# Optimization experiments

Measured on AMD Instinct MI355X. Metric: run time of the kernel, lower is better.

The kernel has to match this reference:

```python
import jax, jax.numpy as jnp
import numpy as np

IN_FEATURES = 4096
OUT_FEATURES = 4096


def setup_inputs() -> dict:
    key = jax.random.key(0)
    k1, k2 = jax.random.split(key)
    x = jax.random.normal(k1, (4, 2048, IN_FEATURES), dtype=jnp.float32)
    latent_weight = jax.random.normal(k2, (OUT_FEATURES, IN_FEATURES), dtype=jnp.float32) * 0.02
    return {"x": x, "latent_weight": latent_weight}


def _quantize(w):
    # abs-mean scale, ternary {-alpha, 0, alpha} with threshold 0.5*alpha
    alpha = jnp.mean(jnp.abs(w))
    threshold = 0.5 * alpha
    return jnp.where(w > threshold, alpha, jnp.where(w < -threshold, -alpha, jnp.zeros_like(w)))


def reference(x, latent_weight):
    qw = _quantize(latent_weight.astype(jnp.float32))
    # F.linear: x @ qw.T  -> [B, S, out_features]
    out = jnp.einsum('bsi,oi->bso', x.astype(jnp.float32), qw)
    return out.astype(x.dtype)
```

## Files before the change

kernel.cpp:

```cpp
#include <hip/hip_runtime.h>
#include <hip/hip_bf16.h>
#include <stdint.h>

#define M_DIM 8192
#define K_DIM 4096
#define N_DIM 4096

typedef __attribute__((ext_vector_type(8))) short short8;
typedef __attribute__((ext_vector_type(4))) float f32x4;

__device__ __forceinline__ void lds_load16(const ushort* g, ushort* l) {
    __builtin_amdgcn_global_load_lds(
        (const __attribute__((address_space(1))) uint32_t*)g,
        (__attribute__((address_space(3))) uint32_t*)l, 16, 0, 0);
}

__device__ __forceinline__ ushort f2bf_rne(float f) {
    uint32_t u = __float_as_uint(f);
    uint32_t r = (u + 0x7FFFu + ((u >> 16) & 1u)) >> 16;
    return (ushort)r;
}

__global__ void k_prep(const float* __restrict__ w, double* __restrict__ partial,
                       const float* __restrict__ x, ushort* __restrict__ xb) {
    const int nth = gridDim.x * blockDim.x;
    const int gtid = blockIdx.x * blockDim.x + threadIdx.x;

    const float4* w4 = (const float4*)w;
    double s = 0.0;
    for (int i = gtid; i < (K_DIM * N_DIM) / 4; i += nth) {
        float4 v = w4[i];
        s += (double)fabsf(v.x) + (double)fabsf(v.y) + (double)fabsf(v.z) + (double)fabsf(v.w);
    }
    #pragma unroll
    for (int off = 32; off > 0; off >>= 1) s += __shfl_down(s, off, 64);
    __shared__ double sm[4];
    int lane = threadIdx.x & 63, wv = threadIdx.x >> 6;
    if (lane == 0) sm[wv] = s;
    __syncthreads();
    if (threadIdx.x == 0) partial[blockIdx.x] = sm[0] + sm[1] + sm[2] + sm[3];

    const float4* x4 = (const float4*)x;
    ushort4* xb4 = (ushort4*)xb;
    for (int i = gtid; i < (M_DIM * K_DIM) / 4; i += nth) {
        float4 v = x4[i];
        ushort4 o;
        o.x = f2bf_rne(v.x);
        o.y = f2bf_rne(v.y);
        o.z = f2bf_rne(v.z);
        o.w = f2bf_rne(v.w);
        xb4[i] = o;
    }
}

__global__ void k_alpha(const double* __restrict__ partial, float* __restrict__ alpha_out) {
    double s = 0.0;
    for (int i = threadIdx.x; i < 2048; i += 256) s += partial[i];
    #pragma unroll
    for (int off = 32; off > 0; off >>= 1) s += __shfl_down(s, off, 64);
    __shared__ double sm[4];
    int lane = threadIdx.x & 63, wv = threadIdx.x >> 6;
    if (lane == 0) sm[wv] = s;
    __syncthreads();
    if (threadIdx.x == 0) {
        double total = sm[0] + sm[1] + sm[2] + sm[3];
        alpha_out[0] = (float)(total * (1.0 / 16777216.0));
    }
}

__global__ void k_quant(const float* __restrict__ w, const float* __restrict__ alpha_p,
                        ushort* __restrict__ qw) {
    const float thr = 0.5f * alpha_p[0];
    const int nth = gridDim.x * blockDim.x;
    const int gtid = blockIdx.x * blockDim.x + threadIdx.x;
    const float4* w4 = (const float4*)w;
    short8* q8 = (short8*)qw;
    for (int i = gtid; i < (K_DIM * N_DIM) / 8; i += nth) {
        float4 a = w4[2 * i], b = w4[2 * i + 1];
        short8 o;
        o[0] = a.x > thr ? (short)0x3F80 : (a.x < -thr ? (short)0xBF80 : (short)0);
        o[1] = a.y > thr ? (short)0x3F80 : (a.y < -thr ? (short)0xBF80 : (short)0);
        o[2] = a.z > thr ? (short)0x3F80 : (a.z < -thr ? (short)0xBF80 : (short)0);
        o[3] = a.w > thr ? (short)0x3F80 : (a.w < -thr ? (short)0xBF80 : (short)0);
        o[4] = b.x > thr ? (short)0x3F80 : (b.x < -thr ? (short)0xBF80 : (short)0);
        o[5] = b.y > thr ? (short)0x3F80 : (b.y < -thr ? (short)0xBF80 : (short)0);
        o[6] = b.z > thr ? (short)0x3F80 : (b.z < -thr ? (short)0xBF80 : (short)0);
        o[7] = b.w > thr ? (short)0x3F80 : (b.w < -thr ? (short)0xBF80 : (short)0);
        q8[i] = o;
    }
}

#define NT (K_DIM / 64)

#define MFMA16(a, b, c) __builtin_amdgcn_mfma_f32_16x16x32_bf16((a), (b), (c), 0, 0, 0)

__global__ __launch_bounds__(512, 2) void k_gemm(const ushort* __restrict__ A,
                                                 const ushort* __restrict__ B,
                                                 const float* __restrict__ alpha_p,
                                                 float* __restrict__ C) {
    __shared__ __align__(16) ushort lds[65536];

    const int tid = threadIdx.x;
    const int lane = tid & 63;
    const int w = tid >> 6;
    const int wr = w >> 2;
    const int wc = w & 3;
    const int r = lane & 15, q = lane >> 4;

    const int wg = blockIdx.x;
    const int swz = (wg & 7) * 64 + (wg >> 3);
    const int bm = swz >> 4;
    const int bn = swz & 15;

    float alpha = alpha_p[0];
    asm volatile("" :: "v"(alpha));

    const ushort* Abase = A + (size_t)bm * 256 * K_DIM;
    const ushort* Bbase = B + (size_t)bn * 256 * K_DIM;

    const int srow = tid >> 3;
    const int sch = (tid & 7) ^ (srow & 7);

    const int ch0 = q ^ (r & 7);
    const int o0 = r * 64 + ch0 * 8;
    const int o1 = r * 64 + (ch0 ^ 4) * 8;

    f32x4 acc[8][4] = {};

    auto SA = [&](int h, int bb, int tt) {
        const ushort* g = Abase + (size_t)(h * 128 + srow) * K_DIM + tt * 64 + sch * 8;
        ushort* l = lds + bb * 32768 + h * 8192 + tid * 8;
        lds_load16(g, l);
        lds_load16(g + (size_t)64 * K_DIM, l + 4096);
    };
    auto SB = [&](int h, int bb, int tt) {
        const ushort* g = Bbase + (size_t)(h * 128 + srow) * K_DIM + tt * 64 + sch * 8;
        ushort* l = lds + bb * 32768 + 16384 + h * 8192 + tid * 8;
        lds_load16(g, l);
        lds_load16(g + (size_t)64 * K_DIM, l + 4096);
    };

    SA(0, 0, 0); SA(1, 0, 0); SB(0, 0, 0); SB(1, 0, 0);
    SB(0, 1, 1); SB(1, 1, 1);
    SA(0, 1, 1); SA(1, 1, 1);
    asm volatile("s_waitcnt vmcnt(8)" ::: "memory");
    __builtin_amdgcn_s_barrier();

    for (int t = 0; t < NT; ++t) {
        const int b = t & 1;
        const ushort* aL = lds + b * 32768 + wr * 8192;
        const ushort* bL = lds + b * 32768 + 16384 + (wc >> 1) * 8192 + (wc & 1) * 4096;
        short8 am[4][2], b01[2][2], b23[2][2];

        #pragma unroll
        for (int i = 0; i < 4; ++i) {
            am[i][0] = *(const short8*)(aL + i * 1024 + o0);
            am[i][1] = *(const short8*)(aL + i * 1024 + o1);
        }
        #pragma unroll
        for (int j = 0; j < 2; ++j) {
            b01[j][0] = *(const short8*)(bL + j * 1024 + o0);
            b01[j][1] = *(const short8*)(bL + j * 1024 + o1);
        }
        asm volatile("s_waitcnt lgkmcnt(8)" ::: "memory");
        __builtin_amdgcn_s_barrier();
        asm volatile("s_waitcnt lgkmcnt(0)" ::: "memory");
        __builtin_amdgcn_sched_barrier(0);
        __builtin_amdgcn_s_setprio(1);
        #pragma unroll
        for (int i = 0; i < 4; ++i)
            #pragma unroll
            for (int j = 0; j < 2; ++j) {
                acc[i][j] = MFMA16(am[i][0], b01[j][0], acc[i][j]);
                acc[i][j] = MFMA16(am[i][1], b01[j][1], acc[i][j]);
            }
        __builtin_amdgcn_s_setprio(0);
        __builtin_amdgcn_s_barrier();

        #pragma unroll
        for (int j = 0; j < 2; ++j) {
            b23[j][0] = *(const short8*)(bL + (2 + j) * 1024 + o0);
            b23[j][1] = *(const short8*)(bL + (2 + j) * 1024 + o1);
        }
        __builtin_amdgcn_s_barrier();
        asm volatile("s_waitcnt lgkmcnt(0)" ::: "memory");
        __builtin_amdgcn_sched_barrier(0);
        __builtin_amdgcn_s_setprio(1);
        #pragma unroll
        for (int i = 0; i < 4; ++i)
            #pragma unroll
            for (int j = 0; j < 2; ++j) {
                acc[i][2 + j] = MFMA16(am[i][0], b23[j][0], acc[i][2 + j]);
                acc[i][2 + j] = MFMA16(am[i][1], b23[j][1], acc[i][2 + j]);
            }
        __builtin_amdgcn_s_setprio(0);
        __builtin_amdgcn_s_barrier();

        #pragma unroll
        for (int i = 0; i < 4; ++i) {
            am[i][0] = *(const short8*)(aL + (4 + i) * 1024 + o0);
            am[i][1] = *(const short8*)(aL + (4 + i) * 1024 + o1);
        }
        if (t + 2 < NT) { SB(0, b, t + 2); SB(1, b, t + 2); }
        __builtin_amdgcn_s_barrier();
        asm volatile("s_waitcnt lgkmcnt(0)" ::: "memory");
        __builtin_amdgcn_sched_barrier(0);
        __builtin_amdgcn_s_setprio(1);
        #pragma unroll
        for (int i = 0; i < 4; ++i)
            #pragma unroll
            for (int j = 0; j < 2; ++j) {
                acc[4 + i][2 + j] = MFMA16(am[i][0], b23[j][0], acc[4 + i][2 + j]);
                acc[4 + i][2 + j] = MFMA16(am[i][1], b23[j][1], acc[4 + i][2 + j]);
            }
        __builtin_amdgcn_s_setprio(0);
        __builtin_amdgcn_s_barrier();

        if (t + 2 < NT) { SA(0, b, t + 2); SA(1, b, t + 2); }
        __builtin_amdgcn_s_setprio(1);
        #pragma unroll
        for (int i = 0; i < 4; ++i)
            #pragma unroll
            for (int j = 0; j < 2; ++j) {
                acc[4 + i][j] = MFMA16(am[i][0], b01[j][0], acc[4 + i][j]);
                acc[4 + i][j] = MFMA16(am[i][1], b01[j][1], acc[4 + i][j]);
            }
        __builtin_amdgcn_s_setprio(0);
        if (t + 2 < NT) asm volatile("s_waitcnt vmcnt(8)" ::: "memory");
        else            asm volatile("s_waitcnt vmcnt(0)" ::: "memory");
        __builtin_amdgcn_s_barrier();
    }

    const int row0 = bm * 256 + wr * 128 + q * 4;
    const int col0 = bn * 256 + wc * 64 + r;
    #pragma unroll
    for (int i = 0; i < 8; ++i)
        #pragma unroll
        for (int j = 0; j < 4; ++j)
            #pragma unroll
            for (int v = 0; v < 4; ++v)
                C[(size_t)(row0 + i * 16 + v) * N_DIM + col0 + j * 16] = alpha * acc[i][j][v];
}

extern "C" void kernel_launch(void* const* d_in, const int* in_sizes, int n_in,
                              void* d_out, int out_size, void* d_ws, size_t ws_size,
                              hipStream_t stream) {
    const float* x = (const float*)d_in[0];
    const float* w = (const float*)d_in[1];
    float* out = (float*)d_out;

    char* ws = (char*)d_ws;
    double* partial = (double*)ws;
    float* alpha = (float*)(ws + 16384);
    ushort* qw = (ushort*)(ws + 32768);
    ushort* xb = (ushort*)(ws + 32768 + (size_t)K_DIM * N_DIM * 2);

    k_prep<<<2048, 256, 0, stream>>>(w, partial, x, xb);
    k_alpha<<<1, 256, 0, stream>>>(partial, alpha);
    k_quant<<<2048, 256, 0, stream>>>(w, alpha, qw);

    k_gemm<<<512, 512, 0, stream>>>(xb, qw, alpha, out);
}
```

Baseline: 509.7 us.

## Software-pipeline LDS fragment loads across K iterations with register double buffering

Restructures the GEMM main loop so the A and B fragments for the next K tile are read from LDS during the current tile's MFMA phases. Separate register sets (amA/amB) replace the single reused fragment array, and the explicit lgkmcnt waits plus several barriers are removed so LDS reads overlap with matrix math. In exchange it uses more VGPRs and changes the global-load wait from vmcnt(8) to vmcnt(0) mid-iteration. That can expose global load latency and weakens the reasoning about ordering between async global-to-LDS writes and the reads.

```diff
diff --git a/kernel.cpp b/kernel.cpp
--- a/kernel.cpp
+++ b/kernel.cpp
@@ -126,6 +126,8 @@
     const int o1 = r * 64 + (ch0 ^ 4) * 8;
 
     f32x4 acc[8][4] = {};
+    short8 amA[4][2], amB[4][2];
+    short8 b01[2][2], b23[2][2];
 
     auto SA = [&](int h, int bb, int tt) {
         const ushort* g = Abase + (size_t)(h * 128 + srow) * K_DIM + tt * 64 + sch * 8;
@@ -141,93 +143,103 @@
     };
 
     SA(0, 0, 0); SA(1, 0, 0); SB(0, 0, 0); SB(1, 0, 0);
-    SB(0, 1, 1); SB(1, 1, 1);
-    SA(0, 1, 1); SA(1, 1, 1);
+    SB(0, 1, 1); SB(1, 1, 1); SA(0, 1, 1); SA(1, 1, 1);
     asm volatile("s_waitcnt vmcnt(8)" ::: "memory");
     __builtin_amdgcn_s_barrier();
+    {
+        const ushort* aL0 = lds + wr * 8192;
+        const ushort* bL0 = lds + 16384 + (wc >> 1) * 8192 + (wc & 1) * 4096;
+        #pragma unroll
+        for (int i = 0; i < 4; ++i) {
+            amA[i][0] = *(const short8*)(aL0 + i * 1024 + o0);
+            amA[i][1] = *(const short8*)(aL0 + i * 1024 + o1);
+        }
+        #pragma unroll
+        for (int j = 0; j < 2; ++j) {
+            b01[j][0] = *(const short8*)(bL0 + j * 1024 + o0);
+            b01[j][1] = *(const short8*)(bL0 + j * 1024 + o1);
+        }
+    }
 
     for (int t = 0; t < NT; ++t) {
         const int b = t & 1;
-        const ushort* aL = lds + b * 32768 + wr * 8192;
-        const ushort* bL = lds + b * 32768 + 16384 + (wc >> 1) * 8192 + (wc & 1) * 4096;
-        short8 am[4][2], b01[2][2], b23[2][2];
-
-        #pragma unroll
-        for (int i = 0; i < 4; ++i) {
-            am[i][0] = *(const short8*)(aL + i * 1024 + o0);
-            am[i][1] = *(const short8*)(aL + i * 1024 + o1);
-        }
-        #pragma unroll
-        for (int j = 0; j < 2; ++j) {
-            b01[j][0] = *(const short8*)(bL + j * 1024 + o0);
-            b01[j][1] = *(const short8*)(bL + j * 1024 + o1);
-        }
-        asm volatile("s_waitcnt lgkmcnt(8)" ::: "memory");
-        __builtin_amdgcn_s_barrier();
-        asm volatile("s_waitcnt lgkmcnt(0)" ::: "memory");
-        __builtin_amdgcn_sched_barrier(0);
-        __builtin_amdgcn_s_setprio(1);
-        #pragma unroll
-        for (int i = 0; i < 4; ++i)
-            #pragma unroll
-            for (int j = 0; j < 2; ++j) {
-                acc[i][j] = MFMA16(am[i][0], b01[j][0], acc[i][j]);
-                acc[i][j] = MFMA16(am[i][1], b01[j][1], acc[i][j]);
-            }
-        __builtin_amdgcn_s_setprio(0);
-        __builtin_amdgcn_s_barrier();
+        const ushort* aL  = lds + b * 32768 + wr * 8192;
+        const ushort* bL  = lds + b * 32768 + 16384 + (wc >> 1) * 8192 + (wc & 1) * 4096;
+        const ushort* aLn = lds + (b ^ 1) * 32768 + wr * 8192;
+        const ushort* bLn = lds + (b ^ 1) * 32768 + 16384 + (wc >> 1) * 8192 + (wc & 1) * 4096;
 
         #pragma unroll
         for (int j = 0; j < 2; ++j) {
             b23[j][0] = *(const short8*)(bL + (2 + j) * 1024 + o0);
             b23[j][1] = *(const short8*)(bL + (2 + j) * 1024 + o1);
         }
-        __builtin_amdgcn_s_barrier();
-        asm volatile("s_waitcnt lgkmcnt(0)" ::: "memory");
         __builtin_amdgcn_sched_barrier(0);
         __builtin_amdgcn_s_setprio(1);
         #pragma unroll
         for (int i = 0; i < 4; ++i)
             #pragma unroll
             for (int j = 0; j < 2; ++j) {
-                acc[i][2 + j] = MFMA16(am[i][0], b23[j][0], acc[i][2 + j]);
-                acc[i][2 + j] = MFMA16(am[i][1], b23[j][1], acc[i][2 + j]);
+                acc[i][j] = MFMA16(amA[i][0], b01[j][0], acc[i][j]);
+                acc[i][j] = MFMA16(amA[i][1], b01[j][1], acc[i][j]);
             }
         __builtin_amdgcn_s_setprio(0);
         __builtin_amdgcn_s_barrier();
 
         #pragma unroll
         for (int i = 0; i < 4; ++i) {
-            am[i][0] = *(const short8*)(aL + (4 + i) * 1024 + o0);
-            am[i][1] = *(const short8*)(aL + (4 + i) * 1024 + o1);
+            amB[i][0] = *(const short8*)(aL + (4 + i) * 1024 + o0);
+            amB[i][1] = *(const short8*)(aL + (4 + i) * 1024 + o1);
+        }
+        __builtin_amdgcn_sched_barrier(0);
+        __builtin_amdgcn_s_setprio(1);
+        #pragma unroll
+        for (int i = 0; i < 4; ++i)
+            #pragma unroll
+            for (int j = 0; j < 2; ++j) {
+                acc[i][2 + j] = MFMA16(amA[i][0], b23[j][0], acc[i][2 + j]);
+                acc[i][2 + j] = MFMA16(amA[i][1], b23[j][1], acc[i][2 + j]);
+            }
+        __builtin_amdgcn_s_setprio(0);
+        asm volatile("s_waitcnt vmcnt(0)" ::: "memory");
+        __builtin_amdgcn_s_barrier();
+
+        if (t + 1 < NT) {
+            #pragma unroll
+            for (int i = 0; i < 4; ++i) {
+                amA[i][0] = *(const short8*)(aLn + i * 1024 + o0);
+                amA[i][1] = *(const short8*)(aLn + i * 1024 + o1);
+            }
         }
         if (t + 2 < NT) { SB(0, b, t + 2); SB(1, b, t + 2); }
-        __builtin_amdgcn_s_barrier();
-        asm volatile("s_waitcnt lgkmcnt(0)" ::: "memory");
         __builtin_amdgcn_sched_barrier(0);
         __builtin_amdgcn_s_setprio(1);
         #pragma unroll
         for (int i = 0; i < 4; ++i)
             #pragma unroll
             for (int j = 0; j < 2; ++j) {
-                acc[4 + i][2 + j] = MFMA16(am[i][0], b23[j][0], acc[4 + i][2 + j]);
-                acc[4 + i][2 + j] = MFMA16(am[i][1], b23[j][1], acc[4 + i][2 + j]);
-            }
-        __builtin_amdgcn_s_setprio(0);
-        __builtin_amdgcn_s_barrier();
-
+                acc[4 + i][2 + j] = MFMA16(amB[i][0], b23[j][0], acc[4 + i][2 + j]);
+                acc[4 + i][2 + j] = MFMA16(amB[i][1], b23[j][1], acc[4 + i][2 + j]);
+            }
+        __builtin_amdgcn_s_setprio(0);
+        __builtin_amdgcn_s_barrier();
+
+        __builtin_amdgcn_s_setprio(1);
+        #pragma unroll
+        for (int i = 0; i < 4; ++i)
+            #pragma unroll
+            for (int j = 0; j < 2; ++j) {
+                acc[4 + i][j] = MFMA16(amB[i][0], b01[j][0], acc[4 + i][j]);
+                acc[4 + i][j] = MFMA16(amB[i][1], b01[j][1], acc[4 + i][j]);
+            }
+        __builtin_amdgcn_s_setprio(0);
+        if (t + 1 < NT) {
+            #pragma unroll
+            for (int j = 0; j < 2; ++j) {
+                b01[j][0] = *(const short8*)(bLn + j * 1024 + o0);
+                b01[j][1] = *(const short8*)(bLn + j * 1024 + o1);
+            }
+        }
         if (t + 2 < NT) { SA(0, b, t + 2); SA(1, b, t + 2); }
-        __builtin_amdgcn_s_setprio(1);
-        #pragma unroll
-        for (int i = 0; i < 4; ++i)
-            #pragma unroll
-            for (int j = 0; j < 2; ++j) {
-                acc[4 + i][j] = MFMA16(am[i][0], b01[j][0], acc[4 + i][j]);
-                acc[4 + i][j] = MFMA16(am[i][1], b01[j][1], acc[4 + i][j]);
-            }
-        __builtin_amdgcn_s_setprio(0);
-        if (t + 2 < NT) asm volatile("s_waitcnt vmcnt(8)" ::: "memory");
-        else            asm volatile("s_waitcnt vmcnt(0)" ::: "memory");
         __builtin_amdgcn_s_barrier();
     }
 
```

Measured after the change: 505.6 us. About the same (-0.8%).
